# Kernel tuning notes

Measured on AMD Instinct MI355X. Metric: run time of the kernel, lower is better.

The kernel has to match this reference:

```python
import jax, jax.numpy as jnp
import numpy as np

EPS = 1e-5

def conv2d(x, w, stride=1, pad=0, groups=1):
    return jax.lax.conv_general_dilated(
        x, w, (stride, stride), [(pad, pad), (pad, pad)],
        feature_group_count=groups,
        dimension_numbers=('NCHW', 'OIHW', 'NCHW'))

def prelu(x, a):
    return jnp.where(x > 0, x, a[None, :, None, None] * x)

def batchnorm(x, g, b):
    # training-mode BN: batch statistics over N,H,W (biased variance, as torch)
    m = jnp.mean(x, axis=(0, 2, 3), keepdims=True)
    v = jnp.var(x, axis=(0, 2, 3), keepdims=True)
    xhat = (x - m) * jax.lax.rsqrt(v + EPS)
    return xhat * g[None, :, None, None] + b[None, :, None, None]

def setup_inputs() -> dict:
    key = jax.random.key(0)
    ks = jax.random.split(key, 8)
    C_in, C_out, stride = 128, 256, 2
    x = jax.random.normal(ks[0], (32, C_in, 56, 56), dtype=jnp.float32)
    w1 = jax.random.normal(ks[1], (C_out, C_in, 1, 1), dtype=jnp.float32) * 0.05
    w_dw = jax.random.normal(ks[2], (C_out, 1, 3, 3), dtype=jnp.float32) * 0.1
    w3 = jax.random.normal(ks[3], (C_out, C_out, 1, 1), dtype=jnp.float32) * 0.05
    w_adj = jax.random.normal(ks[4], (C_out, C_in, 1, 1), dtype=jnp.float32) * 0.05
    a_init = jnp.full((C_out,), 0.25, dtype=jnp.float32)  # PReLU init
    ones = jnp.ones((C_out,), dtype=jnp.float32)
    zeros = jnp.zeros((C_out,), dtype=jnp.float32)
    return {
        'x': x,
        'w1': w1, 'a1': a_init, 'g1': ones, 'b1': zeros,
        'w_dw': w_dw, 'a2': a_init, 'g2': ones, 'b2': zeros,
        'w3': w3, 'a3': a_init, 'g3': ones, 'b3': zeros,
        'w_adj': w_adj,
    }

def reference(x, w1, a1, g1, b1, w_dw, a2, g2, b2, w3, a3, g3, b3, w_adj):
    stride, C_out = 2, w_dw.shape[0]
    residual = conv2d(x, w_adj, stride=stride)  # full-precision shortcut
    xs = jnp.sign(x)
    # binary 1x1 conv (sign(x) already signed; sign is idempotent)
    out = conv2d(jnp.sign(xs), jnp.sign(w1))
    out = batchnorm(prelu(out, a1), g1, b1)
    # binary depthwise 3x3, stride, pad 1
    out = conv2d(jnp.sign(out), jnp.sign(w_dw), stride=stride, pad=1, groups=C_out)
    out = batchnorm(prelu(out, a2), g2, b2)
    # binary 1x1 conv
    out = conv2d(jnp.sign(out), jnp.sign(w3))
    out = batchnorm(prelu(out, a3), g3, b3)
    return out + residual
```

## Files before the change

### kernel.cpp

```cpp
#include <hip/hip_runtime.h>
#include <stdint.h>

#define NB   32
#define CIN  128
#define COUT 256
#define HH   56
#define WW   56
#define S1   (HH*WW)
#define HO   28
#define WO   28
#define S2   (HO*WO)
#define NS1  (NB*S1)
#define NS2  (NB*S2)
#define TOT2 (NS2*COUT)
#define EPSV 1e-5f

constexpr size_t OFF_XBITS = 0;
constexpr size_t OFF_WB1   = OFF_XBITS + (size_t)NS1*8*4;
constexpr size_t OFF_WB3   = OFF_WB1 + 256*8*4;
constexpr size_t OFF_WDW   = OFF_WB3 + 256*16*4;
constexpr size_t OFF_ACC   = OFF_WDW + 4096;
constexpr size_t OFF_WBADJ = OFF_ACC + 3*256*4*sizeof(int);
constexpr size_t OFF_XG    = OFF_WBADJ + (size_t)COUT*CIN*2;
constexpr size_t OFF_OUT1  = OFF_XG + (size_t)NS2*CIN*2;
constexpr size_t OFF_OUT2  = OFF_OUT1 + (size_t)NS1*COUT;
constexpr size_t OFF_XB2   = OFF_OUT2 + (size_t)TOT2;
constexpr size_t OFF_OUT3  = OFF_XB2 + (size_t)NS2*16*4;

typedef __attribute__((ext_vector_type(8))) short bf16x8;
typedef __attribute__((ext_vector_type(4))) float f32x4;

__device__ __forceinline__ uint32_t f2bf(float v) {
  uint32_t u = __float_as_uint(v);
  return (u + 0x7fffu + ((u >> 16) & 1u)) >> 16;
}

__device__ __forceinline__ void bn_finalize(const int* __restrict__ acc4,
                                            float a, float g, float b, float inv_ns,
                                            float& sc, float& sh) {
  float ps = (float)acc4[0];
  float ng = (float)acc4[1];
  float pq = (float)acc4[2];
  float nq = (float)acc4[3];
  float mean = (ps + a*ng) * inv_ns;
  float ex2  = (pq + a*a*nq) * inv_ns;
  float var  = ex2 - mean*mean;
  float rs   = rsqrtf(var + EPSV);
  sc = rs * g;
  sh = b - mean * sc;
}

__global__ __launch_bounds__(256) void packx_kernel(
    const float* __restrict__ x, uint32_t* __restrict__ xbits,
    uint32_t* __restrict__ xg,
    const float* __restrict__ w1, const float* __restrict__ w3,
    const float* __restrict__ wdw, const float* __restrict__ wadj,
    uint32_t* __restrict__ wb1, uint32_t* __restrict__ wb3,
    int8_t* __restrict__ wdws, uint32_t* __restrict__ wbadj,
    int* __restrict__ accbase) {
  int wdx = blockIdx.y;
  if (wdx == 0 && blockIdx.x < 256 && threadIdx.x < 64) {
    int co = blockIdx.x;
    int l  = threadIdx.x;
    if (l < 12) {
      int set = l >> 2, k = l & 3;
      accbase[set*1024 + co*4 + k] = 0;
    }
    for (int h = 0; h < 2; ++h) {
      float v = w1[(size_t)co*CIN + h*64 + l];
      unsigned long long bp = __ballot(v > 0.f);
      unsigned long long bn = __ballot(v < 0.f);
      if (l == 0) {
        wb1[co*8 + 2*h    ] = (uint32_t)bp;
        wb1[co*8 + 2*h + 1] = (uint32_t)(bp >> 32);
        wb1[co*8 + 4 + 2*h    ] = (uint32_t)bn;
        wb1[co*8 + 4 + 2*h + 1] = (uint32_t)(bn >> 32);
      }
    }
    for (int h = 0; h < 4; ++h) {
      float v = w3[(size_t)co*COUT + h*64 + l];
      unsigned long long bp = __ballot(v > 0.f);
      unsigned long long bn = __ballot(v < 0.f);
      if (l == 0) {
        wb3[co*16 + 2*h    ] = (uint32_t)bp;
        wb3[co*16 + 2*h + 1] = (uint32_t)(bp >> 32);
        wb3[co*16 + 8 + 2*h    ] = (uint32_t)bn;
        wb3[co*16 + 8 + 2*h + 1] = (uint32_t)(bn >> 32);
      }
    }
    if (l < 9) {
      float v = wdw[co*9 + l];
      wdws[co*9 + l] = (int8_t)((v > 0.f) - (v < 0.f));
    }
    {
      float v0 = wadj[(size_t)co*CIN + 2*l];
      float v1 = wadj[(size_t)co*CIN + 2*l + 1];
      wbadj[co*64 + l] = f2bf(v0) | (f2bf(v1) << 16);
    }
  }

  int m = blockIdx.x*256 + threadIdx.x;
  int n = m / S1, hw = m % S1;
  size_t base = ((size_t)n*CIN + wdx*32)*S1 + hw;
  uint32_t p = 0, q = 0;
  uint32_t bv[16];
  #pragma unroll
  for (int j = 0; j < 32; ++j) {
    float v = x[base + (size_t)j*S1];
    p |= (uint32_t)(v > 0.f) << j;
    q |= (uint32_t)(v < 0.f) << j;
    uint32_t b = f2bf(v);
    if (j & 1) bv[j >> 1] |= b << 16; else bv[j >> 1] = b;
  }
  xbits[(size_t)m*8 + wdx    ] = p;
  xbits[(size_t)m*8 + 4 + wdx] = q;
  int h = hw / WW, w = hw % WW;
  if (((h | w) & 1) == 0) {
    int m2 = n*S2 + (h >> 1)*WO + (w >> 1);
    uint4* dst = (uint4*)(xg + (size_t)m2*64 + wdx*16);
    dst[0] = make_uint4(bv[0],  bv[1],  bv[2],  bv[3]);
    dst[1] = make_uint4(bv[4],  bv[5],  bv[6],  bv[7]);
    dst[2] = make_uint4(bv[8],  bv[9],  bv[10], bv[11]);
    dst[3] = make_uint4(bv[12], bv[13], bv[14], bv[15]);
  }
}

__global__ __launch_bounds__(256) void conv1_kernel(
    const uint32_t* __restrict__ xb, const uint32_t* __restrict__ wb,
    int8_t* __restrict__ out1, int* __restrict__ accum1) {
  int tid = threadIdx.x;
  int qm = blockIdx.x*256 + tid;
  int m0 = qm*4;
  int n  = m0 / S1;
  int hw0 = m0 - n*S1;
  int co0 = blockIdx.y * 8;

  const uint4* xw = (const uint4*)(xb + (size_t)m0*8);
  uint4 xp0 = xw[0], xq0 = xw[1];
  uint4 xp1 = xw[2], xq1 = xw[3];
  uint4 xp2 = xw[4], xq2 = xw[5];
  uint4 xp3 = xw[6], xq3 = xw[7];

  uint32_t nzw = (xp0.x|xq0.x)&(xp0.y|xq0.y)&(xp0.z|xq0.z)&(xp0.w|xq0.w)
               & (xp1.x|xq1.x)&(xp1.y|xq1.y)&(xp1.z|xq1.z)&(xp1.w|xq1.w)
               & (xp2.x|xq2.x)&(xp2.y|xq2.y)&(xp2.z|xq2.z)&(xp2.w|xq2.w)
               & (xp3.x|xq3.x)&(xp3.y|xq3.y)&(xp3.z|xq3.z)&(xp3.w|xq3.w);
  bool allnz = (nzw == 0xffffffffu);

  __shared__ int sl[256][17];
  __shared__ int sW[4][16];
  uint32_t res[8];
  int stp[8], stn[8], stpq[8], stnq[8];

  #pragma unroll
  for (int j = 0; j < 8; ++j) {
    const uint32_t* w8 = wb + (size_t)(co0 + j)*8;
    uint32_t w0 = w8[0], w1 = w8[1], w2 = w8[2], w3 = w8[3];
    int A0,A1,A2,A3;
#define XORDOT(i,A) A = 128 - 2*(__popc(xp##i.x^w0)+__popc(xp##i.y^w1)+__popc(xp##i.z^w2)+__popc(xp##i.w^w3));
    XORDOT(0,A0) XORDOT(1,A1) XORDOT(2,A2) XORDOT(3,A3)
#undef XORDOT
    if (!allnz) {
#define ZCORR(i,A) { \
      uint32_t z0 = ~(xp##i.x|xq##i.x), z1 = ~(xp##i.y|xq##i.y); \
      uint32_t z2 = ~(xp##i.z|xq##i.z), z3 = ~(xp##i.w|xq##i.w); \
      A += 2*(__popc(z0&w0)+__popc(z1&w1)+__popc(z2&w2)+__popc(z3&w3)) \
         - (__popc(z0)+__popc(z1)+__popc(z2)+__popc(z3)); }
      ZCORR(0,A0) ZCORR(1,A1) ZCORR(2,A2) ZCORR(3,A3)
#undef ZCORR
    }
    if (A0 > 127) A0 = 127;
    if (A1 > 127) A1 = 127;
    if (A2 > 127) A2 = 127;
    if (A3 > 127) A3 = 127;
    res[j] = (uint32_t)(uint8_t)A0 | ((uint32_t)(uint8_t)A1 << 8)
           | ((uint32_t)(uint8_t)A2 << 16) | ((uint32_t)(uint8_t)A3 << 24);
    int ps = 0, ns = 0, pq = 0, nq = 0;
#define STAT(A) if (A > 0) { ps += A; pq += A*A; } else { ns += A; nq += A*A; }
    STAT(A0) STAT(A1) STAT(A2) STAT(A3)
#undef STAT
    stp[j] = ps; stn[j] = ns; stpq[j] = pq; stnq[j] = nq;
  }

  #pragma unroll
  for (int j = 0; j < 4; ++j) {
    sl[tid][j*4+0] = stp[j];  sl[tid][j*4+1] = stn[j];
    sl[tid][j*4+2] = stpq[j]; sl[tid][j*4+3] = stnq[j];
  }
  __syncthreads();

  #pragma unroll
  for (int j = 0; j < 8; ++j)
    *(uint32_t*)(out1 + (size_t)(n*COUT + co0 + j)*S1 + hw0) = res[j];

  int s16 = tid & 15, ch = tid >> 4;
  {
    int part = 0;
    #pragma unroll
    for (int i = 0; i < 16; ++i) part += sl[ch + 16*i][s16];
    part += __shfl_xor(part, 16);
    part += __shfl_xor(part, 32);
    if ((tid & 63) < 16) sW[tid >> 6][s16] = part;
  }
  __syncthreads();
  if (tid < 16) {
    int tot = sW[0][tid] + sW[1][tid] + sW[2][tid] + sW[3][tid];
    atomicAdd(&accum1[co0*4 + tid], tot);
  }

  #pragma unroll
  for (int j = 0; j < 4; ++j) {
    sl[tid][j*4+0] = stp[4+j];  sl[tid][j*4+1] = stn[4+j];
    sl[tid][j*4+2] = stpq[4+j]; sl[tid][j*4+3] = stnq[4+j];
  }
  __syncthreads();
  {
    int part = 0;
    #pragma unroll
    for (int i = 0; i < 16; ++i) part += sl[ch + 16*i][s16];
    part += __shfl_xor(part, 16);
    part += __shfl_xor(part, 32);
    if ((tid & 63) < 16) sW[tid >> 6][s16] = part;
  }
  __syncthreads();
  if (tid < 16) {
    int tot = sW[0][tid] + sW[1][tid] + sW[2][tid] + sW[3][tid];
    atomicAdd(&accum1[co0*4 + 16 + tid], tot);
  }
}

#define DW_SLABS 8
#define DW_RB    68
__global__ __launch_bounds__(256) void dw_kernel(
    const int8_t* __restrict__ out1, const int8_t* __restrict__ wdws,
    const int* __restrict__ acc1, const float* __restrict__ a1,
    const float* __restrict__ g1, const float* __restrict__ b1,
    int8_t* __restrict__ out2, int* __restrict__ accum2) {
  __shared__ int8_t sl[DW_SLABS][57][DW_RB];
  __shared__ int sTp[DW_SLABS], sTn[DW_SLABS], sAcc[DW_SLABS][4];
  int tid = threadIdx.x;
  int nc0 = blockIdx.x * DW_SLABS;
  int co0 = nc0 & (COUT-1);

  int* slw = (int*)&sl[0][0][0];
  #pragma unroll
  for (int i = tid; i < DW_SLABS*57*DW_RB/4; i += 256) slw[i] = 0;
  if (tid < DW_SLABS) { sTp[tid] = 128; sTn[tid] = -129; }
  if (tid < DW_SLABS*4) sAcc[tid >> 2][tid & 3] = 0;
  __syncthreads();

  {
    int slab = tid >> 5;
    int co = co0 + slab;
    float av = a1[co], sc, sh;
    bn_finalize(acc1 + co*4, av, g1[co], b1[co], 1.f/NS1, sc, sh);
    int tp = 128, tn = -129;
    int v0 = -128 + (tid & 31)*8;
    #pragma unroll
    for (int k = 0; k < 8; ++k) {
      int v = v0 + k;
      float f = (float)v;
      float pr = f > 0.f ? f : av*f;
      float tv = pr*sc + sh;
      if (tv > 0.f && v < tp) tp = v;
      if (tv < 0.f && v > tn) tn = v;
    }
    atomicMin(&sTp[slab], tp);
    atomicMax(&sTn[slab], tn);
  }
  __syncthreads();

  for (int i = tid; i < DW_SLABS*784; i += 256) {
    int slab = i / 784;
    int d    = i - slab*784;
    int ih   = d / 14;
    int iwd  = d - ih*14;
    int Tp = sTp[slab], Tn = sTn[slab];
    uint32_t v4 = ((const uint32_t*)(out1 + (size_t)(nc0 + slab)*S1))[d];
    uint32_t s4 = 0;
    #pragma unroll
    for (int k = 0; k < 4; ++k) {
      int v = (int)(int8_t)(v4 >> (8*k));
      int s = (v >= Tp) - (v <= Tn);
      s4 |= (uint32_t)(s & 0xff) << (8*k);
    }
    *(uint32_t*)&sl[slab][ih + 1][4 + 4*iwd] = s4;
  }
  __syncthreads();

  int psum = 0, nsum = 0, psq = 0, nsq = 0;
  int slabD = tid / HO;
  if (tid < DW_SLABS*HO) {
    int ho   = tid - slabD*HO;
    int nc = nc0 + slabD;
    int co = co0 + slabD;
    int wv[9];
    #pragma unroll
    for (int k = 0; k < 9; ++k) wv[k] = wdws[co*9 + k];
    const uint32_t* r0 = (const uint32_t*)&sl[slabD][2*ho    ][4];
    const uint32_t* r1 = (const uint32_t*)&sl[slabD][2*ho + 1][4];
    const uint32_t* r2 = (const uint32_t*)&sl[slabD][2*ho + 2][4];
    uint32_t* o32 = (uint32_t*)(out2 + (size_t)nc*S2 + ho*WO);
    int c0 = 0, c1 = 0, c2 = 0;
    uint32_t obuf = 0;
    #pragma unroll
    for (int q = 0; q < 14; ++q) {
      uint32_t d0 = r0[q], d1 = r1[q], d2 = r2[q];
      int s00=(int)(int8_t)d0, s01=(int)(int8_t)(d0>>8), s02=(int)(int8_t)(d0>>16), s03=(int)(int8_t)(d0>>24);
      int s10=(int)(int8_t)d1, s11=(int)(int8_t)(d1>>8), s12=(int)(int8_t)(d1>>16), s13=(int)(int8_t)(d1>>24);
      int s20=(int)(int8_t)d2, s21=(int)(int8_t)(d2>>8), s22=(int)(int8_t)(d2>>16), s23=(int)(int8_t)(d2>>24);
      int a0 = c0*wv[0] + s00*wv[1] + s01*wv[2]
             + c1*wv[3] + s10*wv[4] + s11*wv[5]
             + c2*wv[6] + s20*wv[7] + s21*wv[8];
      int a1v = s01*wv[0] + s02*wv[1] + s03*wv[2]
              + s11*wv[3] + s12*wv[4] + s13*wv[5]
              + s21*wv[6] + s22*wv[7] + s23*wv[8];
      c0 = s03; c1 = s13; c2 = s23;
      if (a0 > 0) { psum += a0; psq += a0*a0; } else { nsum += a0; nsq += a0*a0; }
      if (a1v > 0) { psum += a1v; psq += a1v*a1v; } else { nsum += a1v; nsq += a1v*a1v; }
      if ((q & 1) == 0) {
        obuf = (uint32_t)(a0 & 0xff) | ((uint32_t)(a1v & 0xff) << 8);
      } else {
        obuf |= ((uint32_t)(a0 & 0xff) << 16) | ((uint32_t)(a1v & 0xff) << 24);
        o32[q >> 1] = obuf;
      }
    }
    atomicAdd(&sAcc[slabD][0], psum);
    atomicAdd(&sAcc[slabD][1], nsum);
    atomicAdd(&sAcc[slabD][2], psq);
    atomicAdd(&sAcc[slabD][3], nsq);
  }
  __syncthreads();

  if (tid < DW_SLABS*4) {
    int slab = tid >> 2, k = tid & 3;
    atomicAdd(&accum2[(co0 + slab)*4 + k], sAcc[slab][k]);
  }
}

__global__ __launch_bounds__(256) void pack2_kernel(
    const int8_t* __restrict__ out2, const int* __restrict__ acc2,
    const float* __restrict__ a2, const float* __restrict__ g2,
    const float* __restrict__ b2, uint32_t* __restrict__ xb2) {
  __shared__ int sTp[32], sTn[32];
  int wdx = blockIdx.y;
  if (threadIdx.x < 32) {
    int c = wdx*32 + threadIdx.x;
    float av = a2[c], sc, sh;
    bn_finalize(acc2 + c*4, av, g2[c], b2[c], 1.f/NS2, sc, sh);
    int tp = 10, tn = -10;
    for (int v = -9; v <= 9; ++v) {
      float f = (float)v;
      float pr = f > 0.f ? f : av*f;
      float tv = pr*sc + sh;
      if (tv > 0.f && v < tp) tp = v;
      if (tv < 0.f && v > tn) tn = v;
    }
    sTp[threadIdx.x] = tp; sTn[threadIdx.x] = tn;
  }
  __syncthreads();
  int m = blockIdx.x*256 + threadIdx.x;
  int n = m / S2, hw = m % S2;
  uint32_t p = 0, q = 0;
  #pragma unroll
  for (int j = 0; j < 32; ++j) {
    int c = wdx*32 + j;
    int v = out2[(size_t)(n*COUT + c)*S2 + hw];
    p |= (uint32_t)(v >= sTp[j]) << j;
    q |= (uint32_t)(v <= sTn[j]) << j;
  }
  xb2[(size_t)m*16 + wdx    ] = p;
  xb2[(size_t)m*16 + 8 + wdx] = q;
}

__global__ __launch_bounds__(256) void conv3_kernel(
    const uint32_t* __restrict__ xb2, const uint32_t* __restrict__ wb3,
    int16_t* __restrict__ out3, int* __restrict__ accum3) {
  int tid = threadIdx.x;
  int qm = blockIdx.x*256 + tid;
  int m0 = qm*2;
  int co0 = blockIdx.y * 8;

  const uint4* xw = (const uint4*)(xb2 + (size_t)m0*16);
  uint4 P0a = xw[0], P0b = xw[1], Q0a = xw[2], Q0b = xw[3];
  uint4 P1a = xw[4], P1b = xw[5], Q1a = xw[6], Q1b = xw[7];

  uint32_t nz = (P0a.x|Q0a.x)&(P0a.y|Q0a.y)&(P0a.z|Q0a.z)&(P0a.w|Q0a.w)
              & (P0b.x|Q0b.x)&(P0b.y|Q0b.y)&(P0b.z|Q0b.z)&(P0b.w|Q0b.w)
              & (P1a.x|Q1a.x)&(P1a.y|Q1a.y)&(P1a.z|Q1a.z)&(P1a.w|Q1a.w)
              & (P1b.x|Q1b.x)&(P1b.y|Q1b.y)&(P1b.z|Q1b.z)&(P1b.w|Q1b.w);

  uint32_t m0w[4], m1w[4];
  __shared__ int sl[256][33];

  if (nz == 0xffffffffu) {
    #pragma unroll
    for (int j = 0; j < 8; ++j) {
      const uint32_t* w = wb3 + (size_t)(co0 + j)*16;
      int s0 = __popc(P0a.x^w[0])+__popc(P0a.y^w[1])+__popc(P0a.z^w[2])+__popc(P0a.w^w[3])
             + __popc(P0b.x^w[4])+__popc(P0b.y^w[5])+__popc(P0b.z^w[6])+__popc(P0b.w^w[7]);
      int s1 = __popc(P1a.x^w[0])+__popc(P1a.y^w[1])+__popc(P1a.z^w[2])+__popc(P1a.w^w[3])
             + __popc(P1b.x^w[4])+__popc(P1b.y^w[5])+__popc(P1b.z^w[6])+__popc(P1b.w^w[7]);
      int a0 = 256 - 2*s0, a1 = 256 - 2*s1;
      if ((j & 1) == 0) {
        m0w[j >> 1] = (uint32_t)(uint16_t)(int16_t)a0;
        m1w[j >> 1] = (uint32_t)(uint16_t)(int16_t)a1;
      } else {
        m0w[j >> 1] |= (uint32_t)(uint16_t)(int16_t)a0 << 16;
        m1w[j >> 1] |= (uint32_t)(uint16_t)(int16_t)a1 << 16;
      }
      int ps = 0, ns = 0, pq = 0, nq = 0;
      if (a0 > 0) { ps += a0; pq += a0*a0; } else { ns += a0; nq += a0*a0; }
      if (a1 > 0) { ps += a1; pq += a1*a1; } else { ns += a1; nq += a1*a1; }
      sl[tid][j*4+0] = ps; sl[tid][j*4+1] = ns;
      sl[tid][j*4+2] = pq; sl[tid][j*4+3] = nq;
    }
  } else {
    #pragma unroll
    for (int j = 0; j < 8; ++j) {
      const uint32_t* w = wb3 + (size_t)(co0 + j)*16;
      int a0 = __popc(P0a.x&w[0])+__popc(P0a.y&w[1])+__popc(P0a.z&w[2])+__popc(P0a.w&w[3])
             + __popc(P0b.x&w[4])+__popc(P0b.y&w[5])+__popc(P0b.z&w[6])+__popc(P0b.w&w[7])
             + __popc(Q0a.x&w[8])+__popc(Q0a.y&w[9])+__popc(Q0a.z&w[10])+__popc(Q0a.w&w[11])
             + __popc(Q0b.x&w[12])+__popc(Q0b.y&w[13])+__popc(Q0b.z&w[14])+__popc(Q0b.w&w[15])
             - __popc(P0a.x&w[8])-__popc(P0a.y&w[9])-__popc(P0a.z&w[10])-__popc(P0a.w&w[11])
             - __popc(P0b.x&w[12])-__popc(P0b.y&w[13])-__popc(P0b.z&w[14])-__popc(P0b.w&w[15])
             - __popc(Q0a.x&w[0])-__popc(Q0a.y&w[1])-__popc(Q0a.z&w[2])-__popc(Q0a.w&w[3])
             - __popc(Q0b.x&w[4])-__popc(Q0b.y&w[5])-__popc(Q0b.z&w[6])-__popc(Q0b.w&w[7]);
      int a1 = __popc(P1a.x&w[0])+__popc(P1a.y&w[1])+__popc(P1a.z&w[2])+__popc(P1a.w&w[3])
             + __popc(P1b.x&w[4])+__popc(P1b.y&w[5])+__popc(P1b.z&w[6])+__popc(P1b.w&w[7])
             + __popc(Q1a.x&w[8])+__popc(Q1a.y&w[9])+__popc(Q1a.z&w[10])+__popc(Q1a.w&w[11])
             + __popc(Q1b.x&w[12])+__popc(Q1b.y&w[13])+__popc(Q1b.z&w[14])+__popc(Q1b.w&w[15])
             - __popc(P1a.x&w[8])-__popc(P1a.y&w[9])-__popc(P1a.z&w[10])-__popc(P1a.w&w[11])
             - __popc(P1b.x&w[12])-__popc(P1b.y&w[13])-__popc(P1b.z&w[14])-__popc(P1b.w&w[15])
             - __popc(Q1a.x&w[0])-__popc(Q1a.y&w[1])-__popc(Q1a.z&w[2])-__popc(Q1a.w&w[3])
             - __popc(Q1b.x&w[4])-__popc(Q1b.y&w[5])-__popc(Q1b.z&w[6])-__popc(Q1b.w&w[7]);
      if ((j & 1) == 0) {
        m0w[j >> 1] = (uint32_t)(uint16_t)(int16_t)a0;
        m1w[j >> 1] = (uint32_t)(uint16_t)(int16_t)a1;
      } else {
        m0w[j >> 1] |= (uint32_t)(uint16_t)(int16_t)a0 << 16;
        m1w[j >> 1] |= (uint32_t)(uint16_t)(int16_t)a1 << 16;
      }
      int ps = 0, ns = 0, pq = 0, nq = 0;
      if (a0 > 0) { ps += a0; pq += a0*a0; } else { ns += a0; nq += a0*a0; }
      if (a1 > 0) { ps += a1; pq += a1*a1; } else { ns += a1; nq += a1*a1; }
      sl[tid][j*4+0] = ps; sl[tid][j*4+1] = ns;
      sl[tid][j*4+2] = pq; sl[tid][j*4+3] = nq;
    }
  }
  __syncthreads();

  *(uint4*)&out3[(size_t)m0*COUT + co0]       = make_uint4(m0w[0], m0w[1], m0w[2], m0w[3]);
  *(uint4*)&out3[(size_t)(m0+1)*COUT + co0]   = make_uint4(m1w[0], m1w[1], m1w[2], m1w[3]);

  int s = tid & 31, g = tid >> 5;
  int part = 0;
  #pragma unroll
  for (int i = 0; i < 32; ++i) part += sl[g + 8*i][s];
  part += __shfl_xor(part, 32);
  __shared__ int sW[4][32];
  if ((tid & 63) < 32) sW[tid >> 6][s] = part;
  __syncthreads();
  if (tid < 32) {
    int tot = sW[0][tid] + sW[1][tid] + sW[2][tid] + sW[3][tid];
    atomicAdd(&accum3[co0*4 + tid], tot);
  }
}

__global__ __launch_bounds__(256) void resfinal_kernel(
    const uint16_t* __restrict__ xg, const uint16_t* __restrict__ wb,
    const int16_t* __restrict__ out3,
    const float* __restrict__ a3, const float* __restrict__ g3,
    const float* __restrict__ b3, const int* __restrict__ acc3,
    float* __restrict__ out) {
  __shared__ float scs[256], shs[256], avs[256];
  int tid = threadIdx.x;
  {
    float sc, sh;
    bn_finalize(acc3 + tid*4, a3[tid], g3[tid], b3[tid], 1.f/NS2, sc, sh);
    scs[tid] = sc; shs[tid] = sh; avs[tid] = a3[tid];
  }
  __syncthreads();

  int lane = tid & 63;
  int wid  = tid >> 6;
  int m0  = blockIdx.x*64 + wid*16;
  int r16 = lane & 15, hi = lane >> 4;
  int koff = hi * 8;

  const bf16x8* arow = (const bf16x8*)(xg + (size_t)(m0 + r16)*CIN + koff);
  bf16x8 af0 = arow[0], af1 = arow[4], af2 = arow[8], af3 = arow[12];

  f32x4 dd[16];
  #pragma unroll
  for (int t = 0; t < 16; ++t) {
    const bf16x8* brow = (const bf16x8*)(wb + (size_t)(t*16 + r16)*CIN + koff);
    f32x4 a = {0.f,0.f,0.f,0.f};
    a = __builtin_amdgcn_mfma_f32_16x16x32_bf16(af0, brow[0],  a, 0,0,0);
    a = __builtin_amdgcn_mfma_f32_16x16x32_bf16(af1, brow[4],  a, 0,0,0);
    a = __builtin_amdgcn_mfma_f32_16x16x32_bf16(af2, brow[8],  a, 0,0,0);
    a = __builtin_amdgcn_mfma_f32_16x16x32_bf16(af3, brow[12], a, 0,0,0);
    dd[t] = a;
  }

  int mrow = m0 + hi*4;
  int n  = mrow / S2;
  int hw = mrow - n*S2;
  #pragma unroll
  for (int t = 0; t < 16; ++t) {
    int co = t*16 + r16;
    float av = avs[co], sc = scs[co], sh = shs[co];
    size_t o = ((size_t)n*COUT + co)*S2 + hw;
    #pragma unroll
    for (int r = 0; r < 4; ++r) {
      float f = (float)out3[(size_t)(mrow + r)*COUT + co];
      float pp = f > 0.f ? f : av*f;
      out[o + r] = pp*sc + sh + dd[t][r];
    }
  }
}

extern "C" void kernel_launch(void* const* d_in, const int* in_sizes, int n_in,
                              void* d_out, int out_size, void* d_ws, size_t ws_size,
                              hipStream_t stream) {
  (void)in_sizes; (void)n_in; (void)out_size; (void)ws_size;
  const float* x    = (const float*)d_in[0];
  const float* w1   = (const float*)d_in[1];
  const float* a1   = (const float*)d_in[2];
  const float* g1   = (const float*)d_in[3];
  const float* b1   = (const float*)d_in[4];
  const float* wdw  = (const float*)d_in[5];
  const float* a2   = (const float*)d_in[6];
  const float* g2   = (const float*)d_in[7];
  const float* b2   = (const float*)d_in[8];
  const float* w3   = (const float*)d_in[9];
  const float* a3   = (const float*)d_in[10];
  const float* g3   = (const float*)d_in[11];
  const float* b3   = (const float*)d_in[12];
  const float* wadj = (const float*)d_in[13];
  float* out = (float*)d_out;

  char* ws = (char*)d_ws;
  uint32_t* xbits = (uint32_t*)(ws + OFF_XBITS);
  uint32_t* wb1   = (uint32_t*)(ws + OFF_WB1);
  uint32_t* wb3   = (uint32_t*)(ws + OFF_WB3);
  int8_t*   wdws  = (int8_t*)  (ws + OFF_WDW);
  int*      acc1  = (int*)     (ws + OFF_ACC);
  int*      acc2  = acc1 + 256*4;
  int*      acc3  = acc2 + 256*4;
  uint32_t* wbadj = (uint32_t*)(ws + OFF_WBADJ);
  uint32_t* xg    = (uint32_t*)(ws + OFF_XG);
  int8_t*   out1  = (int8_t*)  (ws + OFF_OUT1);
  int8_t*   out2  = (int8_t*)  (ws + OFF_OUT2);
  uint32_t* xb2   = (uint32_t*)(ws + OFF_XB2);
  int16_t*  out3  = (int16_t*) (ws + OFF_OUT3);

  packx_kernel<<<dim3(NS1/256, 4), 256, 0, stream>>>(
      x, xbits, xg, w1, w3, wdw, wadj, wb1, wb3, wdws, wbadj, acc1);
  conv1_kernel<<<dim3(NS1/1024, 32), 256, 0, stream>>>(xbits, wb1, out1, acc1);
  dw_kernel<<<NB*COUT/DW_SLABS, 256, 0, stream>>>(out1, wdws, acc1, a1, g1, b1, out2, acc2);
  pack2_kernel<<<dim3(NS2/256, 8), 256, 0, stream>>>(out2, acc2, a2, g2, b2, xb2);
  conv3_kernel<<<dim3(NS2/512, 32), 256, 0, stream>>>(xb2, wb3, out3, acc3);
  resfinal_kernel<<<NS2/64, 256, 0, stream>>>(
      (const uint16_t*)xg, (const uint16_t*)wbadj, out3, a3, g3, b3, acc3, out);
}
```

Baseline: 113.1 us.

## Fuse six stage kernels into one cooperative persistent kernel with grid syncs

Converts the six stage kernels into device functions and runs them inside a single cooperative persistent kernel, looping over virtual blocks and separating stages with grid-wide syncs. The goal is to remove per-kernel launch gaps and tail drain between stages. In exchange it caps concurrent blocks to occupancy (a launch bound of 3 blocks per CU and a shared 34KB LDS buffer), which may lower occupancy for the lighter stages, and it adds host-side attribute and occupancy queries on every call. The six separate kernels remain as a fallback when cooperative launch is unavailable.

```diff
diff --git a/kernel.cpp b/kernel.cpp
--- a/kernel.cpp
+++ b/kernel.cpp
@@ -1,5 +1,8 @@
 #include <hip/hip_runtime.h>
+#include <hip/hip_cooperative_groups.h>
 #include <stdint.h>
+
+namespace cg = cooperative_groups;
 
 #define NB   32
 #define CIN  128
@@ -50,74 +53,82 @@
   sh = b - mean * sc;
 }
 
-__global__ __launch_bounds__(256) void packx_kernel(
-    const float* __restrict__ x, uint32_t* __restrict__ xbits,
-    uint32_t* __restrict__ xg,
-    const float* __restrict__ w1, const float* __restrict__ w3,
-    const float* __restrict__ wdw, const float* __restrict__ wadj,
-    uint32_t* __restrict__ wb1, uint32_t* __restrict__ wb3,
-    int8_t* __restrict__ wdws, uint32_t* __restrict__ wbadj,
-    int* __restrict__ accbase) {
-  int wdx = blockIdx.y;
-  if (wdx == 0 && blockIdx.x < 256 && threadIdx.x < 64) {
-    int co = blockIdx.x;
-    int l  = threadIdx.x;
+struct MegaArgs {
+  const float *x, *w1, *a1, *g1, *b1, *wdw, *a2, *g2, *b2, *w3, *a3, *g3, *b3, *wadj;
+  float* out;
+  uint32_t *xbits, *wb1, *wb3;
+  int8_t *wdws;
+  int *acc1, *acc2, *acc3;
+  uint32_t *wbadj, *xg;
+  int8_t *out1, *out2;
+  uint32_t *xb2;
+  int16_t *out3;
+};
+
+#define DW_SLABS 8
+#define DW_RB    68
+
+
+__device__ __forceinline__ void packx_body(
+    int bx, int wdx, int tid, const MegaArgs& A) {
+  if (wdx == 0 && bx < 256 && tid < 64) {
+    int co = bx, l = tid;
     if (l < 12) {
       int set = l >> 2, k = l & 3;
-      accbase[set*1024 + co*4 + k] = 0;
+      A.acc1[set*1024 + co*4 + k] = 0;
     }
     for (int h = 0; h < 2; ++h) {
-      float v = w1[(size_t)co*CIN + h*64 + l];
+      float v = A.w1[(size_t)co*CIN + h*64 + l];
       unsigned long long bp = __ballot(v > 0.f);
       unsigned long long bn = __ballot(v < 0.f);
       if (l == 0) {
-        wb1[co*8 + 2*h    ] = (uint32_t)bp;
-        wb1[co*8 + 2*h + 1] = (uint32_t)(bp >> 32);
-        wb1[co*8 + 4 + 2*h    ] = (uint32_t)bn;
-        wb1[co*8 + 4 + 2*h + 1] = (uint32_t)(bn >> 32);
+        A.wb1[co*8 + 2*h    ] = (uint32_t)bp;
+        A.wb1[co*8 + 2*h + 1] = (uint32_t)(bp >> 32);
+        A.wb1[co*8 + 4 + 2*h    ] = (uint32_t)bn;
+        A.wb1[co*8 + 4 + 2*h + 1] = (uint32_t)(bn >> 32);
       }
     }
     for (int h = 0; h < 4; ++h) {
-      float v = w3[(size_t)co*COUT + h*64 + l];
+      float v = A.w3[(size_t)co*COUT + h*64 + l];
       unsigned long long bp = __ballot(v > 0.f);
       unsigned long long bn = __ballot(v < 0.f);
       if (l == 0) {
-        wb3[co*16 + 2*h    ] = (uint32_t)bp;
-        wb3[co*16 + 2*h + 1] = (uint32_t)(bp >> 32);
-        wb3[co*16 + 8 + 2*h    ] = (uint32_t)bn;
-        wb3[co*16 + 8 + 2*h + 1] = (uint32_t)(bn >> 32);
+        A.wb3[co*16 + 2*h    ] = (uint32_t)bp;
+        A.wb3[co*16 + 2*h + 1] = (uint32_t)(bp >> 32);
+        A.wb3[co*16 + 8 + 2*h    ] = (uint32_t)bn;
+        A.wb3[co*16 + 8 + 2*h + 1] = (uint32_t)(bn >> 32);
       }
     }
     if (l < 9) {
-      float v = wdw[co*9 + l];
-      wdws[co*9 + l] = (int8_t)((v > 0.f) - (v < 0.f));
+      float v = A.wdw[co*9 + l];
+      A.wdws[co*9 + l] = (int8_t)((v > 0.f) - (v < 0.f));
     }
     {
-      float v0 = wadj[(size_t)co*CIN + 2*l];
-      float v1 = wadj[(size_t)co*CIN + 2*l + 1];
-      wbadj[co*64 + l] = f2bf(v0) | (f2bf(v1) << 16);
-    }
-  }
-
-  int m = blockIdx.x*256 + threadIdx.x;
+      float v0 = A.wadj[(size_t)co*CIN + 2*l];
+      float v1 = A.wadj[(size_t)co*CIN + 2*l + 1];
+      A.wbadj[co*64 + l] = f2bf(v0) | (f2bf(v1) << 16);
+    }
+  }
+
+  int m = bx*256 + tid;
   int n = m / S1, hw = m % S1;
   size_t base = ((size_t)n*CIN + wdx*32)*S1 + hw;
   uint32_t p = 0, q = 0;
   uint32_t bv[16];
   #pragma unroll
   for (int j = 0; j < 32; ++j) {
-    float v = x[base + (size_t)j*S1];
+    float v = A.x[base + (size_t)j*S1];
     p |= (uint32_t)(v > 0.f) << j;
     q |= (uint32_t)(v < 0.f) << j;
     uint32_t b = f2bf(v);
     if (j & 1) bv[j >> 1] |= b << 16; else bv[j >> 1] = b;
   }
-  xbits[(size_t)m*8 + wdx    ] = p;
-  xbits[(size_t)m*8 + 4 + wdx] = q;
+  A.xbits[(size_t)m*8 + wdx    ] = p;
+  A.xbits[(size_t)m*8 + 4 + wdx] = q;
   int h = hw / WW, w = hw % WW;
   if (((h | w) & 1) == 0) {
     int m2 = n*S2 + (h >> 1)*WO + (w >> 1);
-    uint4* dst = (uint4*)(xg + (size_t)m2*64 + wdx*16);
+    uint4* dst = (uint4*)(A.xg + (size_t)m2*64 + wdx*16);
     dst[0] = make_uint4(bv[0],  bv[1],  bv[2],  bv[3]);
     dst[1] = make_uint4(bv[4],  bv[5],  bv[6],  bv[7]);
     dst[2] = make_uint4(bv[8],  bv[9],  bv[10], bv[11]);
@@ -125,17 +136,17 @@
   }
 }
 
-__global__ __launch_bounds__(256) void conv1_kernel(
-    const uint32_t* __restrict__ xb, const uint32_t* __restrict__ wb,
-    int8_t* __restrict__ out1, int* __restrict__ accum1) {
-  int tid = threadIdx.x;
-  int qm = blockIdx.x*256 + tid;
+__device__ __forceinline__ void conv1_body(
+    int bx, int coy, int tid, char* smem, const MegaArgs& A) {
+  int (*sl)[17] = (int(*)[17])smem;
+  int (*sW)[16] = (int(*)[16])(smem + 17408);
+  int qm = bx*256 + tid;
   int m0 = qm*4;
   int n  = m0 / S1;
   int hw0 = m0 - n*S1;
-  int co0 = blockIdx.y * 8;
-
-  const uint4* xw = (const uint4*)(xb + (size_t)m0*8);
+  int co0 = coy * 8;
+
+  const uint4* xw = (const uint4*)(A.xbits + (size_t)m0*8);
   uint4 xp0 = xw[0], xq0 = xw[1];
   uint4 xp1 = xw[2], xq1 = xw[3];
   uint4 xp2 = xw[4], xq2 = xw[5];
@@ -147,25 +158,23 @@
                & (xp3.x|xq3.x)&(xp3.y|xq3.y)&(xp3.z|xq3.z)&(xp3.w|xq3.w);
   bool allnz = (nzw == 0xffffffffu);
 
-  __shared__ int sl[256][17];
-  __shared__ int sW[4][16];
   uint32_t res[8];
   int stp[8], stn[8], stpq[8], stnq[8];
 
   #pragma unroll
   for (int j = 0; j < 8; ++j) {
-    const uint32_t* w8 = wb + (size_t)(co0 + j)*8;
+    const uint32_t* w8 = A.wb1 + (size_t)(co0 + j)*8;
     uint32_t w0 = w8[0], w1 = w8[1], w2 = w8[2], w3 = w8[3];
     int A0,A1,A2,A3;
-#define XORDOT(i,A) A = 128 - 2*(__popc(xp##i.x^w0)+__popc(xp##i.y^w1)+__popc(xp##i.z^w2)+__popc(xp##i.w^w3));
+#define XORDOT(i,Av) Av = 128 - 2*(__popc(xp##i.x^w0)+__popc(xp##i.y^w1)+__popc(xp##i.z^w2)+__popc(xp##i.w^w3));
     XORDOT(0,A0) XORDOT(1,A1) XORDOT(2,A2) XORDOT(3,A3)
 #undef XORDOT
     if (!allnz) {
-#define ZCORR(i,A) { \
+#define ZCORR(i,Av) { \
       uint32_t z0 = ~(xp##i.x|xq##i.x), z1 = ~(xp##i.y|xq##i.y); \
       uint32_t z2 = ~(xp##i.z|xq##i.z), z3 = ~(xp##i.w|xq##i.w); \
-      A += 2*(__popc(z0&w0)+__popc(z1&w1)+__popc(z2&w2)+__popc(z3&w3)) \
-         - (__popc(z0)+__popc(z1)+__popc(z2)+__popc(z3)); }
+      Av += 2*(__popc(z0&w0)+__popc(z1&w1)+__popc(z2&w2)+__popc(z3&w3)) \
+          - (__popc(z0)+__popc(z1)+__popc(z2)+__popc(z3)); }
       ZCORR(0,A0) ZCORR(1,A1) ZCORR(2,A2) ZCORR(3,A3)
 #undef ZCORR
     }
@@ -176,7 +185,7 @@
     res[j] = (uint32_t)(uint8_t)A0 | ((uint32_t)(uint8_t)A1 << 8)
            | ((uint32_t)(uint8_t)A2 << 16) | ((uint32_t)(uint8_t)A3 << 24);
     int ps = 0, ns = 0, pq = 0, nq = 0;
-#define STAT(A) if (A > 0) { ps += A; pq += A*A; } else { ns += A; nq += A*A; }
+#define STAT(Av) if (Av > 0) { ps += Av; pq += Av*Av; } else { ns += Av; nq += Av*Av; }
     STAT(A0) STAT(A1) STAT(A2) STAT(A3)
 #undef STAT
     stp[j] = ps; stn[j] = ns; stpq[j] = pq; stnq[j] = nq;
@@ -191,7 +200,7 @@
 
   #pragma unroll
   for (int j = 0; j < 8; ++j)
-    *(uint32_t*)(out1 + (size_t)(n*COUT + co0 + j)*S1 + hw0) = res[j];
+    *(uint32_t*)(A.out1 + (size_t)(n*COUT + co0 + j)*S1 + hw0) = res[j];
 
   int s16 = tid & 15, ch = tid >> 4;
   {
@@ -205,7 +214,7 @@
   __syncthreads();
   if (tid < 16) {
     int tot = sW[0][tid] + sW[1][tid] + sW[2][tid] + sW[3][tid];
-    atomicAdd(&accum1[co0*4 + tid], tot);
+    atomicAdd(&A.acc1[co0*4 + tid], tot);
   }
 
   #pragma unroll
@@ -225,24 +234,21 @@
   __syncthreads();
   if (tid < 16) {
     int tot = sW[0][tid] + sW[1][tid] + sW[2][tid] + sW[3][tid];
-    atomicAdd(&accum1[co0*4 + 16 + tid], tot);
-  }
-}
-
-#define DW_SLABS 8
-#define DW_RB    68
-__global__ __launch_bounds__(256) void dw_kernel(
-    const int8_t* __restrict__ out1, const int8_t* __restrict__ wdws,
-    const int* __restrict__ acc1, const float* __restrict__ a1,
-    const float* __restrict__ g1, const float* __restrict__ b1,
-    int8_t* __restrict__ out2, int* __restrict__ accum2) {
-  __shared__ int8_t sl[DW_SLABS][57][DW_RB];
-  __shared__ int sTp[DW_SLABS], sTn[DW_SLABS], sAcc[DW_SLABS][4];
-  int tid = threadIdx.x;
-  int nc0 = blockIdx.x * DW_SLABS;
+    atomicAdd(&A.acc1[co0*4 + 16 + tid], tot);
+  }
+  __syncthreads();
+}
+
+__device__ __forceinline__ void dw_body(
+    int vb, int tid, char* smem, const MegaArgs& A) {
+  int8_t (*sl)[57][DW_RB] = (int8_t(*)[57][DW_RB])smem;
+  int* sTp  = (int*)(smem + 31008);
+  int* sTn  = (int*)(smem + 31040);
+  int (*sAcc)[4] = (int(*)[4])(smem + 31072);
+  int nc0 = vb * DW_SLABS;
   int co0 = nc0 & (COUT-1);
 
-  int* slw = (int*)&sl[0][0][0];
+  int* slw = (int*)smem;
   #pragma unroll
   for (int i = tid; i < DW_SLABS*57*DW_RB/4; i += 256) slw[i] = 0;
   if (tid < DW_SLABS) { sTp[tid] = 128; sTn[tid] = -129; }
@@ -252,8 +258,8 @@
   {
     int slab = tid >> 5;
     int co = co0 + slab;
-    float av = a1[co], sc, sh;
-    bn_finalize(acc1 + co*4, av, g1[co], b1[co], 1.f/NS1, sc, sh);
+    float av = A.a1[co], sc, sh;
+    bn_finalize(A.acc1 + co*4, av, A.g1[co], A.b1[co], 1.f/NS1, sc, sh);
     int tp = 128, tn = -129;
     int v0 = -128 + (tid & 31)*8;
     #pragma unroll
@@ -276,7 +282,7 @@
     int ih   = d / 14;
     int iwd  = d - ih*14;
     int Tp = sTp[slab], Tn = sTn[slab];
-    uint32_t v4 = ((const uint32_t*)(out1 + (size_t)(nc0 + slab)*S1))[d];
+    uint32_t v4 = ((const uint32_t*)(A.out1 + (size_t)(nc0 + slab)*S1))[d];
     uint32_t s4 = 0;
     #pragma unroll
     for (int k = 0; k < 4; ++k) {
@@ -296,11 +302,11 @@
     int co = co0 + slabD;
     int wv[9];
     #pragma unroll
-    for (int k = 0; k < 9; ++k) wv[k] = wdws[co*9 + k];
+    for (int k = 0; k < 9; ++k) wv[k] = A.wdws[co*9 + k];
     const uint32_t* r0 = (const uint32_t*)&sl[slabD][2*ho    ][4];
     const uint32_t* r1 = (const uint32_t*)&sl[slabD][2*ho + 1][4];
     const uint32_t* r2 = (const uint32_t*)&sl[slabD][2*ho + 2][4];
-    uint32_t* o32 = (uint32_t*)(out2 + (size_t)nc*S2 + ho*WO);
+    uint32_t* o32 = (uint32_t*)(A.out2 + (size_t)nc*S2 + ho*WO);
     int c0 = 0, c1 = 0, c2 = 0;
     uint32_t obuf = 0;
     #pragma unroll
@@ -334,20 +340,19 @@
 
   if (tid < DW_SLABS*4) {
     int slab = tid >> 2, k = tid & 3;
-    atomicAdd(&accum2[(co0 + slab)*4 + k], sAcc[slab][k]);
-  }
-}
-
-__global__ __launch_bounds__(256) void pack2_kernel(
-    const int8_t* __restrict__ out2, const int* __restrict__ acc2,
-    const float* __restrict__ a2, const float* __restrict__ g2,
-    const float* __restrict__ b2, uint32_t* __restrict__ xb2) {
-  __shared__ int sTp[32], sTn[32];
-  int wdx = blockIdx.y;
-  if (threadIdx.x < 32) {
-    int c = wdx*32 + threadIdx.x;
-    float av = a2[c], sc, sh;
-    bn_finalize(acc2 + c*4, av, g2[c], b2[c], 1.f/NS2, sc, sh);
+    atomicAdd(&A.acc2[(co0 + slab)*4 + k], sAcc[slab][k]);
+  }
+  __syncthreads();
+}
+
+__device__ __forceinline__ void pack2_body(
+    int bx, int wdx, int tid, char* smem, const MegaArgs& A) {
+  int* sTp = (int*)smem;
+  int* sTn = (int*)(smem + 128);
+  if (tid < 32) {
+    int c = wdx*32 + tid;
+    float av = A.a2[c], sc, sh;
+    bn_finalize(A.acc2 + c*4, av, A.g2[c], A.b2[c], 1.f/NS2, sc, sh);
     int tp = 10, tn = -10;
     for (int v = -9; v <= 9; ++v) {
       float f = (float)v;
@@ -356,32 +361,33 @@
       if (tv > 0.f && v < tp) tp = v;
       if (tv < 0.f && v > tn) tn = v;
     }
-    sTp[threadIdx.x] = tp; sTn[threadIdx.x] = tn;
-  }
-  __syncthreads();
-  int m = blockIdx.x*256 + threadIdx.x;
+    sTp[tid] = tp; sTn[tid] = tn;
+  }
+  __syncthreads();
+  int m = bx*256 + tid;
   int n = m / S2, hw = m % S2;
   uint32_t p = 0, q = 0;
   #pragma unroll
   for (int j = 0; j < 32; ++j) {
     int c = wdx*32 + j;
-    int v = out2[(size_t)(n*COUT + c)*S2 + hw];
+    int v = A.out2[(size_t)(n*COUT + c)*S2 + hw];
     p |= (uint32_t)(v >= sTp[j]) << j;
     q |= (uint32_t)(v <= sTn[j]) << j;
   }
-  xb2[(size_t)m*16 + wdx    ] = p;
-  xb2[(size_t)m*16 + 8 + wdx] = q;
-}
-
-__global__ __launch_bounds__(256) void conv3_kernel(
-    const uint32_t* __restrict__ xb2, const uint32_t* __restrict__ wb3,
-    int16_t* __restrict__ out3, int* __restrict__ accum3) {
-  int tid = threadIdx.x;
-  int qm = blockIdx.x*256 + tid;
+  A.xb2[(size_t)m*16 + wdx    ] = p;
+  A.xb2[(size_t)m*16 + 8 + wdx] = q;
+  __syncthreads();
+}
+
+__device__ __forceinline__ void conv3_body(
+    int bx, int coy, int tid, char* smem, const MegaArgs& A) {
+  int (*sl)[33] = (int(*)[33])smem;
+  int (*sW)[32] = (int(*)[32])(smem + 33792);
+  int qm = bx*256 + tid;
   int m0 = qm*2;
-  int co0 = blockIdx.y * 8;
-
-  const uint4* xw = (const uint4*)(xb2 + (size_t)m0*16);
+  int co0 = coy * 8;
+
+  const uint4* xw = (const uint4*)(A.xb2 + (size_t)m0*16);
   uint4 P0a = xw[0], P0b = xw[1], Q0a = xw[2], Q0b = xw[3];
   uint4 P1a = xw[4], P1b = xw[5], Q1a = xw[6], Q1b = xw[7];
 
@@ -391,12 +397,10 @@
               & (P1b.x|Q1b.x)&(P1b.y|Q1b.y)&(P1b.z|Q1b.z)&(P1b.w|Q1b.w);
 
   uint32_t m0w[4], m1w[4];
-  __shared__ int sl[256][33];
-
   if (nz == 0xffffffffu) {
     #pragma unroll
     for (int j = 0; j < 8; ++j) {
-      const uint32_t* w = wb3 + (size_t)(co0 + j)*16;
+      const uint32_t* w = A.wb3 + (size_t)(co0 + j)*16;
       int s0 = __popc(P0a.x^w[0])+__popc(P0a.y^w[1])+__popc(P0a.z^w[2])+__popc(P0a.w^w[3])
              + __popc(P0b.x^w[4])+__popc(P0b.y^w[5])+__popc(P0b.z^w[6])+__popc(P0b.w^w[7]);
       int s1 = __popc(P1a.x^w[0])+__popc(P1a.y^w[1])+__popc(P1a.z^w[2])+__popc(P1a.w^w[3])
@@ -418,7 +422,7 @@
   } else {
     #pragma unroll
     for (int j = 0; j < 8; ++j) {
-      const uint32_t* w = wb3 + (size_t)(co0 + j)*16;
+      const uint32_t* w = A.wb3 + (size_t)(co0 + j)*16;
       int a0 = __popc(P0a.x&w[0])+__popc(P0a.y&w[1])+__popc(P0a.z&w[2])+__popc(P0a.w&w[3])
              + __popc(P0b.x&w[4])+__popc(P0b.y&w[5])+__popc(P0b.z&w[6])+__popc(P0b.w&w[7])
              + __popc(Q0a.x&w[8])+__popc(Q0a.y&w[9])+__popc(Q0a.z&w[10])+__popc(Q0a.w&w[11])
@@ -451,51 +455,48 @@
   }
   __syncthreads();
 
-  *(uint4*)&out3[(size_t)m0*COUT + co0]       = make_uint4(m0w[0], m0w[1], m0w[2], m0w[3]);
-  *(uint4*)&out3[(size_t)(m0+1)*COUT + co0]   = make_uint4(m1w[0], m1w[1], m1w[2], m1w[3]);
+  *(uint4*)&A.out3[(size_t)m0*COUT + co0]     = make_uint4(m0w[0], m0w[1], m0w[2], m0w[3]);
+  *(uint4*)&A.out3[(size_t)(m0+1)*COUT + co0] = make_uint4(m1w[0], m1w[1], m1w[2], m1w[3]);
 
   int s = tid & 31, g = tid >> 5;
   int part = 0;
   #pragma unroll
   for (int i = 0; i < 32; ++i) part += sl[g + 8*i][s];
   part += __shfl_xor(part, 32);
-  __shared__ int sW[4][32];
   if ((tid & 63) < 32) sW[tid >> 6][s] = part;
   __syncthreads();
   if (tid < 32) {
     int tot = sW[0][tid] + sW[1][tid] + sW[2][tid] + sW[3][tid];
-    atomicAdd(&accum3[co0*4 + tid], tot);
-  }
-}
-
-__global__ __launch_bounds__(256) void resfinal_kernel(
-    const uint16_t* __restrict__ xg, const uint16_t* __restrict__ wb,
-    const int16_t* __restrict__ out3,
-    const float* __restrict__ a3, const float* __restrict__ g3,
-    const float* __restrict__ b3, const int* __restrict__ acc3,
-    float* __restrict__ out) {
-  __shared__ float scs[256], shs[256], avs[256];
-  int tid = threadIdx.x;
+    atomicAdd(&A.acc3[co0*4 + tid], tot);
+  }
+  __syncthreads();
+}
+
+__device__ __forceinline__ void resfinal_body(
+    int vb, int tid, char* smem, const MegaArgs& A) {
+  float* scs = (float*)smem;
+  float* shs = (float*)(smem + 1024);
+  float* avs = (float*)(smem + 2048);
   {
     float sc, sh;
-    bn_finalize(acc3 + tid*4, a3[tid], g3[tid], b3[tid], 1.f/NS2, sc, sh);
-    scs[tid] = sc; shs[tid] = sh; avs[tid] = a3[tid];
+    bn_finalize(A.acc3 + tid*4, A.a3[tid], A.g3[tid], A.b3[tid], 1.f/NS2, sc, sh);
+    scs[tid] = sc; shs[tid] = sh; avs[tid] = A.a3[tid];
   }
   __syncthreads();
 
   int lane = tid & 63;
   int wid  = tid >> 6;
-  int m0  = blockIdx.x*64 + wid*16;
+  int m0  = vb*64 + wid*16;
   int r16 = lane & 15, hi = lane >> 4;
   int koff = hi * 8;
 
-  const bf16x8* arow = (const bf16x8*)(xg + (size_t)(m0 + r16)*CIN + koff);
+  const bf16x8* arow = (const bf16x8*)((const uint16_t*)A.xg + (size_t)(m0 + r16)*CIN + koff);
   bf16x8 af0 = arow[0], af1 = arow[4], af2 = arow[8], af3 = arow[12];
 
   f32x4 dd[16];
   #pragma unroll
   for (int t = 0; t < 16; ++t) {
-    const bf16x8* brow = (const bf16x8*)(wb + (size_t)(t*16 + r16)*CIN + koff);
+    const bf16x8* brow = (const bf16x8*)((const uint16_t*)A.wbadj + (size_t)(t*16 + r16)*CIN + koff);
     f32x4 a = {0.f,0.f,0.f,0.f};
     a = __builtin_amdgcn_mfma_f32_16x16x32_bf16(af0, brow[0],  a, 0,0,0);
     a = __builtin_amdgcn_mfma_f32_16x16x32_bf16(af1, brow[4],  a, 0,0,0);
@@ -514,54 +515,120 @@
     size_t o = ((size_t)n*COUT + co)*S2 + hw;
     #pragma unroll
     for (int r = 0; r < 4; ++r) {
-      float f = (float)out3[(size_t)(mrow + r)*COUT + co];
+      float f = (float)A.out3[(size_t)(mrow + r)*COUT + co];
       float pp = f > 0.f ? f : av*f;
-      out[o + r] = pp*sc + sh + dd[t][r];
-    }
-  }
+      A.out[o + r] = pp*sc + sh + dd[t][r];
+    }
+  }
+  __syncthreads();
+}
+
+__launch_bounds__(256, 3)
+__global__ void mega_kernel(MegaArgs A) {
+  cg::grid_group grid = cg::this_grid();
+  __shared__ __align__(16) char smem[34816];
+  int tid = threadIdx.x;
+  int nvb = gridDim.x;
+
+  for (int vb = blockIdx.x; vb < 392*4; vb += nvb)
+    packx_body(vb % 392, vb / 392, tid, A);
+  grid.sync();
+
+  for (int vb = blockIdx.x; vb < 98*32; vb += nvb)
+    conv1_body(vb % 98, vb / 98, tid, smem, A);
+  grid.sync();
+
+  for (int vb = blockIdx.x; vb < 1024; vb += nvb)
+    dw_body(vb, tid, smem, A);
+  grid.sync();
+
+  for (int vb = blockIdx.x; vb < 98*8; vb += nvb)
+    pack2_body(vb % 98, vb / 98, tid, smem, A);
+  grid.sync();
+
+  for (int vb = blockIdx.x; vb < 49*32; vb += nvb)
+    conv3_body(vb % 49, vb / 49, tid, smem, A);
+  grid.sync();
+
+  for (int vb = blockIdx.x; vb < 392; vb += nvb)
+    resfinal_body(vb, tid, smem, A);
+}
+
+__global__ __launch_bounds__(256) void packx_kernel(MegaArgs A) {
+  packx_body(blockIdx.x, blockIdx.y, threadIdx.x, A);
+}
+__global__ __launch_bounds__(256) void conv1_kernel(MegaArgs A) {
+  __shared__ __align__(16) char smem[17664];
+  conv1_body(blockIdx.x, blockIdx.y, threadIdx.x, smem, A);
+}
+__global__ __launch_bounds__(256) void dw_kernel(MegaArgs A) {
+  __shared__ __align__(16) char smem[31200];
+  dw_body(blockIdx.x, threadIdx.x, smem, A);
+}
+__global__ __launch_bounds__(256) void pack2_kernel(MegaArgs A) {
+  __shared__ __align__(16) char smem[256];
+  pack2_body(blockIdx.x, blockIdx.y, threadIdx.x, smem, A);
+}
+__global__ __launch_bounds__(256) void conv3_kernel(MegaArgs A) {
+  __shared__ __align__(16) char smem[34304];
+  conv3_body(blockIdx.x, blockIdx.y, threadIdx.x, smem, A);
+}
+__global__ __launch_bounds__(256) void resfinal_kernel(MegaArgs A) {
+  __shared__ __align__(16) char smem[3072];
+  resfinal_body(blockIdx.x, threadIdx.x, smem, A);
 }
 
 extern "C" void kernel_launch(void* const* d_in, const int* in_sizes, int n_in,
                               void* d_out, int out_size, void* d_ws, size_t ws_size,
                               hipStream_t stream) {
   (void)in_sizes; (void)n_in; (void)out_size; (void)ws_size;
-  const float* x    = (const float*)d_in[0];
-  const float* w1   = (const float*)d_in[1];
-  const float* a1   = (const float*)d_in[2];
-  const float* g1   = (const float*)d_in[3];
-  const float* b1   = (const float*)d_in[4];
-  const float* wdw  = (const float*)d_in[5];
-  const float* a2   = (const float*)d_in[6];
-  const float* g2   = (const float*)d_in[7];
-  const float* b2   = (const float*)d_in[8];
-  const float* w3   = (const float*)d_in[9];
-  const float* a3   = (const float*)d_in[10];
-  const float* g3   = (const float*)d_in[11];
-  const float* b3   = (const float*)d_in[12];
-  const float* wadj = (const float*)d_in[13];
-  float* out = (float*)d_out;
-
   char* ws = (char*)d_ws;
-  uint32_t* xbits = (uint32_t*)(ws + OFF_XBITS);
-  uint32_t* wb1   = (uint32_t*)(ws + OFF_WB1);
-  uint32_t* wb3   = (uint32_t*)(ws + OFF_WB3);
-  int8_t*   wdws  = (int8_t*)  (ws + OFF_WDW);
-  int*      acc1  = (int*)     (ws + OFF_ACC);
-  int*      acc2  = acc1 + 256*4;
-  int*      acc3  = acc2 + 256*4;
-  uint32_t* wbadj = (uint32_t*)(ws + OFF_WBADJ);
-  uint32_t* xg    = (uint32_t*)(ws + OFF_XG);
-  int8_t*   out1  = (int8_t*)  (ws + OFF_OUT1);
-  int8_t*   out2  = (int8_t*)  (ws + OFF_OUT2);
-  uint32_t* xb2   = (uint32_t*)(ws + OFF_XB2);
-  int16_t*  out3  = (int16_t*) (ws + OFF_OUT3);
-
-  packx_kernel<<<dim3(NS1/256, 4), 256, 0, stream>>>(
-      x, xbits, xg, w1, w3, wdw, wadj, wb1, wb3, wdws, wbadj, acc1);
-  conv1_kernel<<<dim3(NS1/1024, 32), 256, 0, stream>>>(xbits, wb1, out1, acc1);
-  dw_kernel<<<NB*COUT/DW_SLABS, 256, 0, stream>>>(out1, wdws, acc1, a1, g1, b1, out2, acc2);
-  pack2_kernel<<<dim3(NS2/256, 8), 256, 0, stream>>>(out2, acc2, a2, g2, b2, xb2);
-  conv3_kernel<<<dim3(NS2/512, 32), 256, 0, stream>>>(xb2, wb3, out3, acc3);
-  resfinal_kernel<<<NS2/64, 256, 0, stream>>>(
-      (const uint16_t*)xg, (const uint16_t*)wbadj, out3, a3, g3, b3, acc3, out);
-}
+  MegaArgs A;
+  A.x    = (const float*)d_in[0];
+  A.w1   = (const float*)d_in[1];
+  A.a1   = (const float*)d_in[2];
+  A.g1   = (const float*)d_in[3];
+  A.b1   = (const float*)d_in[4];
+  A.wdw  = (const float*)d_in[5];
+  A.a2   = (const float*)d_in[6];
+  A.g2   = (const float*)d_in[7];
+  A.b2   = (const float*)d_in[8];
+  A.w3   = (const float*)d_in[9];
+  A.a3   = (const float*)d_in[10];
+  A.g3   = (const float*)d_in[11];
+  A.b3   = (const float*)d_in[12];
+  A.wadj = (const float*)d_in[13];
+  A.out  = (float*)d_out;
+  A.xbits = (uint32_t*)(ws + OFF_XBITS);
+  A.wb1   = (uint32_t*)(ws + OFF_WB1);
+  A.wb3   = (uint32_t*)(ws + OFF_WB3);
+  A.wdws  = (int8_t*)  (ws + OFF_WDW);
+  A.acc1  = (int*)     (ws + OFF_ACC);
+  A.acc2  = A.acc1 + 256*4;
+  A.acc3  = A.acc2 + 256*4;
+  A.wbadj = (uint32_t*)(ws + OFF_WBADJ);
+  A.xg    = (uint32_t*)(ws + OFF_XG);
+  A.out1  = (int8_t*)  (ws + OFF_OUT1);
+  A.out2  = (int8_t*)  (ws + OFF_OUT2);
+  A.xb2   = (uint32_t*)(ws + OFF_XB2);
+  A.out3  = (int16_t*) (ws + OFF_OUT3);
+
+  int coop = 0;
+  hipDeviceGetAttribute(&coop, hipDeviceAttributeCooperativeLaunch, 0);
+  int maxBlk = 0;
+  hipOccupancyMaxActiveBlocksPerMultiprocessor(&maxBlk, mega_kernel, 256, 0);
+
+  if (coop && maxBlk > 0) {
+    int grid = maxBlk * 256;
+    if (grid > 1568) grid = 1568;
+    void* args[] = { (void*)&A };
+    hipLaunchCooperativeKernel(mega_kernel, dim3(grid), dim3(256), args, 0, stream);
+  } else {
+    packx_kernel   <<<dim3(NS1/256, 4), 256, 0, stream>>>(A);
+    conv1_kernel   <<<dim3(NS1/1024, 32), 256, 0, stream>>>(A);
+    dw_kernel      <<<NB*COUT/DW_SLABS, 256, 0, stream>>>(A);
+    pack2_kernel   <<<dim3(NS2/256, 8), 256, 0, stream>>>(A);
+    conv3_kernel   <<<dim3(NS2/512, 32), 256, 0, stream>>>(A);
+    resfinal_kernel<<<NS2/64, 256, 0, stream>>>(A);
+  }
+}
```

New measurement: 378.9 us. 235% more time.
